# Kernel tuning notes

Measured on AMD Instinct MI355X. Metric: run time of the kernel, lower is better.

The kernel has to match this reference:

```python
import jax, jax.numpy as jnp
import numpy as np

N = 100_000   # nodes
E = 1_600_000 # edges per edge type
DIN = 128     # input_dim
DH = 128      # prot_hidden_dim
L = 3         # prot_num_layers
EPS = 1e-5


def setup_inputs() -> dict:
    key = jax.random.key(0)
    ks = jax.random.split(key, 8)
    s = 1.0 / np.sqrt(DH)
    return {
        "x": jax.random.normal(ks[0], (N, DIN), jnp.float32),
        "src": jax.random.randint(ks[1], (3, E), 0, N, jnp.int32),
        "dst": jax.random.randint(ks[2], (3, E), 0, N, jnp.int32),
        "gc_W0": jax.random.normal(ks[3], (3, DIN, DH), jnp.float32) * s,
        "gc_b0": jnp.zeros((3, DH), jnp.float32),
        "gc_W": jax.random.normal(ks[4], (L - 1, 3, DH, DH), jnp.float32) * s,
        "gc_b": jnp.zeros((L - 1, 3, DH), jnp.float32),
        "fc_W": jax.random.normal(ks[5], (L, DH, DH), jnp.float32) * s,
        "fc_b": jnp.zeros((L, DH), jnp.float32),
        "bn_gamma": jnp.ones((L, DH), jnp.float32),
        "bn_beta": jnp.zeros((L, DH), jnp.float32),
    }


def _graph_conv(x, src, dst, W, b):
    # DGL GraphConv, norm='both': D_in^{-1/2} A D_out^{-1/2} X W + b
    ones = jnp.ones(src.shape[0], x.dtype)
    deg_out = jnp.clip(jax.ops.segment_sum(ones, src, num_segments=N), 1.0)
    deg_in = jnp.clip(jax.ops.segment_sum(ones, dst, num_segments=N), 1.0)
    # apply weight first (same math; keeps gathered message width = DH)
    h = (x * jax.lax.rsqrt(deg_out)[:, None]) @ W  # [N, DH]
    agg = jax.ops.segment_sum(h[src], dst, num_segments=N)  # gather + scatter-add
    return agg * jax.lax.rsqrt(deg_in)[:, None] + b


def _batchnorm(x, gamma, beta):
    # training-mode BatchNorm1d: biased batch statistics
    mu = jnp.mean(x, axis=0)
    var = jnp.mean(jnp.square(x - mu), axis=0)
    return (x - mu) * jax.lax.rsqrt(var + EPS) * gamma + beta


def reference(x, src, dst, gc_W0, gc_b0, gc_W, gc_b, fc_W, fc_b, bn_gamma, bn_beta):
    h = x
    for l in range(L):
        W = gc_W0 if l == 0 else gc_W[l - 1]
        b = gc_b0 if l == 0 else gc_b[l - 1]
        # HeteroGraphConv with aggregate='sum' over 3 edge types
        out = _graph_conv(h, src[0], dst[0], W[0], b[0])
        for e in range(1, 3):
            out = out + _graph_conv(h, src[e], dst[e], W[e], b[e])
        # FC -> ReLU -> BatchNorm (dropout = identity in eval mode)
        h = _batchnorm(jax.nn.relu(out @ fc_W[l] + fc_b[l]), bn_gamma[l], bn_beta[l])
    return h
```

## Files before the change

### kernel.cpp

```cpp
#include <hip/hip_runtime.h>


#define EPSV 1e-5f
#define CH 4096
#define MAXNB 512

typedef __attribute__((ext_vector_type(8))) short s8v;
typedef __attribute__((ext_vector_type(4))) float f4v;

__global__ void coarse_hist(const int* __restrict__ src, const int* __restrict__ dst,
                            int* __restrict__ chd, int* __restrict__ chs,
                            int E, int NB) {
    __shared__ int hd[MAXNB], hs[MAXNB];
    int t = blockIdx.y;
    for (int i = threadIdx.x; i < MAXNB; i += 256) { hd[i] = 0; hs[i] = 0; }
    __syncthreads();
    int base = blockIdx.x * CH;
    int end = base + CH < E ? base + CH : E;
    const int* sp = src + (size_t)t * E;
    const int* dp = dst + (size_t)t * E;
    for (int i = base + threadIdx.x; i < end; i += 256) {
        atomicAdd(&hd[dp[i] >> 8], 1);
        atomicAdd(&hs[sp[i] >> 8], 1);
    }
    __syncthreads();
    for (int b = threadIdx.x; b < NB; b += 256) {
        if (hd[b]) atomicAdd(&chd[t * NB + b], hd[b]);
        if (hs[b]) atomicAdd(&chs[t * NB + b], hs[b]);
    }
}

__global__ void scan_off(const int* __restrict__ chd, const int* __restrict__ chs,
                         int* __restrict__ offd, int* __restrict__ offs,
                         int* __restrict__ gcd, int* __restrict__ gcs,
                         int* __restrict__ rowptr, int NB, int N, int E) {
    __shared__ int s[MAXNB];
    int tid = threadIdx.x;
    for (int a = 0; a < 6; ++a) {
        const int* h = (a < 3) ? chd + a * NB : chs + (a - 3) * NB;
        int* off = (a < 3) ? offd + a * (NB + 1) : offs + (a - 3) * (NB + 1);
        int* gc = (a < 3) ? gcd + a * NB : gcs + (a - 3) * NB;
        s[tid] = (tid < NB) ? h[tid] : 0;
        __syncthreads();
        for (int o = 1; o < MAXNB; o <<= 1) {
            int v = (tid >= o) ? s[tid - o] : 0;
            __syncthreads();
            s[tid] += v;
            __syncthreads();
        }
        if (tid < NB) {
            off[tid + 1] = s[tid];
            if (tid == 0) off[0] = 0;
        }
        __syncthreads();
        if (tid < NB) gc[tid] = off[tid];
        __syncthreads();
    }
    if (tid < 3) rowptr[tid * (N + 1) + N] = E;
}

__launch_bounds__(256)
__global__ void scatter_coarse(const int* __restrict__ src, const int* __restrict__ dst,
                               int* __restrict__ gcd, int* __restrict__ gcs,
                               int* __restrict__ dbuf, unsigned char* __restrict__ sbuf,
                               int E, int NB) {
    __shared__ int hd[MAXNB], hs[MAXNB];
    __shared__ int lod[MAXNB], los[MAXNB];
    __shared__ int bd[MAXNB], bs[MAXNB];
    __shared__ int rbi[CH];
    __shared__ unsigned char rbs[CH];
    const int tid = threadIdx.x;
    const int t = blockIdx.y;
    const int base = blockIdx.x * CH;
    const int end = base + CH < E ? base + CH : E;
    const int cnt = end - base;
    const int* sp = src + (size_t)t * E;
    const int* dp = dst + (size_t)t * E;

    for (int i = tid; i < MAXNB; i += 256) { hd[i] = 0; hs[i] = 0; }
    __syncthreads();
    for (int i = base + tid; i < end; i += 256) {
        atomicAdd(&hd[dp[i] >> 8], 1);
        atomicAdd(&hs[sp[i] >> 8], 1);
    }
    __syncthreads();
    for (int b = tid; b < NB; b += 256) {
        bd[b] = hd[b] ? atomicAdd(&gcd[t * NB + b], hd[b]) : 0;
        bs[b] = hs[b] ? atomicAdd(&gcs[t * NB + b], hs[b]) : 0;
    }
    lod[tid] = hd[tid]; lod[tid + 256] = hd[tid + 256];
    los[tid] = hs[tid]; los[tid + 256] = hs[tid + 256];
    __syncthreads();
    for (int o = 1; o < MAXNB; o <<= 1) {
        int a0 = lod[tid], a1 = lod[tid + 256];
        int b0 = los[tid], b1 = los[tid + 256];
        int p0 = (tid >= o) ? lod[tid - o] : 0;
        int p1 = lod[tid + 256 - o];
        int q0 = (tid >= o) ? los[tid - o] : 0;
        int q1 = los[tid + 256 - o];
        __syncthreads();
        lod[tid] = a0 + p0; lod[tid + 256] = a1 + p1;
        los[tid] = b0 + q0; los[tid + 256] = b1 + q1;
        __syncthreads();
    }
    hd[tid] = lod[tid] - hd[tid]; hd[tid + 256] = lod[tid + 256] - hd[tid + 256];
    hs[tid] = los[tid] - hs[tid]; hs[tid + 256] = los[tid + 256] - hs[tid + 256];
    __syncthreads();
    for (int i = base + tid; i < end; i += 256) {
        int sv = sp[i], dv = dp[i];
        int lp = atomicAdd(&hd[dv >> 8], 1);
        rbi[lp] = (sv << 8) | (dv & 255);
        int ls = atomicAdd(&hs[sv >> 8], 1);
        rbs[ls] = (unsigned char)(sv & 255);
    }
    __syncthreads();
    for (int i = tid; i < cnt; i += 256) {
        int lo = 0, hi = NB - 1;
        while (lo < hi) { int mid = (lo + hi) >> 1; if (lod[mid] > i) hi = mid; else lo = mid + 1; }
        int excl = lo ? lod[lo - 1] : 0;
        dbuf[(size_t)t * E + bd[lo] + (i - excl)] = rbi[i];
    }
    for (int i = tid; i < cnt; i += 256) {
        int lo = 0, hi = NB - 1;
        while (lo < hi) { int mid = (lo + hi) >> 1; if (los[mid] > i) hi = mid; else lo = mid + 1; }
        int excl = lo ? los[lo - 1] : 0;
        sbuf[(size_t)t * E + bs[lo] + (i - excl)] = rbs[i];
    }
}

__global__ void fine_src(const unsigned char* __restrict__ sbuf, const int* __restrict__ offs,
                         float* __restrict__ dro, int E, int N, int NB) {
    __shared__ int h[256];
    int b = blockIdx.x, t = blockIdx.y;
    int tid = threadIdx.x;
    h[tid] = 0;
    __syncthreads();
    int beg = offs[t * (NB + 1) + b], end = offs[t * (NB + 1) + b + 1];
    const unsigned char* sp = sbuf + (size_t)t * E;
    for (int i = beg + tid; i < end; i += 256) atomicAdd(&h[sp[i]], 1);
    __syncthreads();
    int node = b * 256 + tid;
    if (node < N) {
        int dg = h[tid] < 1 ? 1 : h[tid];
        dro[(size_t)t * N + node] = rsqrtf((float)dg);
    }
}

#define FDCAP 6656
__global__ void fine_dst(const int* __restrict__ dbuf, const int* __restrict__ offd,
                         const float* __restrict__ dro, int* __restrict__ erec,
                         int* __restrict__ rowptr, float* __restrict__ dri,
                         int E, int N, int NB) {
    __shared__ int h[256], sc[256], cur[256];
    __shared__ int rb[FDCAP];
    int b = blockIdx.x, t = blockIdx.y;
    int tid = threadIdx.x;
    h[tid] = 0;
    __syncthreads();
    int beg = offd[t * (NB + 1) + b], end = offd[t * (NB + 1) + b + 1];
    int cnt = end - beg;
    const int* dp = dbuf + (size_t)t * E;
    const float* drt = dro + (size_t)t * N;
    for (int i = beg + tid; i < end; i += 256) atomicAdd(&h[dp[i] & 255], 1);
    __syncthreads();
    sc[tid] = h[tid];
    __syncthreads();
    for (int o = 1; o < 256; o <<= 1) {
        int v = (tid >= o) ? sc[tid - o] : 0;
        __syncthreads();
        sc[tid] += v;
        __syncthreads();
    }
    int excl = sc[tid] - h[tid];
    cur[tid] = excl;
    int node = b * 256 + tid;
    if (node < N) {
        rowptr[t * (N + 1) + node] = beg + excl;
        int dg = h[tid] < 1 ? 1 : h[tid];
        dri[(size_t)t * N + node] = rsqrtf((float)dg);
    }
    __syncthreads();
    if (cnt <= FDCAP) {
        for (int i = beg + tid; i < end; i += 256) {
            int v = dp[i];
            int p = atomicAdd(&cur[v & 255], 1);
            rb[p] = v >> 8;
        }
        __syncthreads();
        for (int i = tid; i < cnt; i += 256) {
            int sv = rb[i];
            int wq = (int)(drt[sv] * 4095.0f + 0.5f);
            erec[(size_t)t * E + beg + i] = sv | (wq << 20);
        }
    } else {
        for (int i = beg + tid; i < end; i += 256) {
            int v = dp[i];
            int sv = v >> 8;
            int wq = (int)(drt[sv] * 4095.0f + 0.5f);
            int p = beg + atomicAdd(&cur[v & 255], 1);
            erec[(size_t)t * E + p] = sv | (wq << 20);
        }
    }
}

__device__ __forceinline__ unsigned int bfr(float f) {
    unsigned int u = __float_as_uint(f);
    return (u + 0x7FFFu + ((u >> 16) & 1u)) >> 16;
}
__device__ __forceinline__ unsigned int pack2(float lo, float hi) {
    return bfr(lo) | (bfr(hi) << 16);
}
__device__ __forceinline__ float blo(unsigned int u) { return __uint_as_float(u << 16); }
__device__ __forceinline__ float bhi(unsigned int u) { return __uint_as_float(u & 0xFFFF0000u); }

__global__ void cvt_bf16(const float* __restrict__ h, unsigned short* __restrict__ h2,
                         int total8) {
    int i = blockIdx.x * 256 + threadIdx.x;
    if (i >= total8) return;
    const float4* hp = (const float4*)h + (size_t)i * 2;
    float4 v0 = hp[0], v1 = hp[1];
    uint4 o;
    o.x = pack2(v0.x, v0.y);
    o.y = pack2(v0.z, v0.w);
    o.z = pack2(v1.x, v1.y);
    o.w = pack2(v1.z, v1.w);
    ((uint4*)h2)[i] = o;
}

__global__ void pack_w(const float* __restrict__ gcW0, const float* __restrict__ gcW,
                       const float* __restrict__ fcW, unsigned short* __restrict__ Wg,
                       unsigned short* __restrict__ Wf) {
    int mat = blockIdx.x;
    const float* srcp;
    unsigned short* dstp;
    if (mat < 9) {
        int l = mat / 3, e = mat % 3;
        srcp = (l == 0) ? gcW0 + (size_t)e * 16384
                        : gcW + ((size_t)(l - 1) * 3 + e) * 16384;
        dstp = Wg + (size_t)mat * 16384;
    } else {
        srcp = fcW + (size_t)(mat - 9) * 16384;
        dstp = Wf + (size_t)(mat - 9) * 16384;
    }
    for (int p = threadIdx.x; p < 16384; p += 256) {
        int j = p & 7;
        int ln = (p >> 3) & 63;
        int nt = (p >> 9) & 7;
        int ks = p >> 12;
        int k = ks * 32 + (ln >> 4) * 8 + j;
        int n = nt * 16 + (ln & 15);
        dstp[p] = (unsigned short)bfr(srcp[k * 128 + n]);
    }
}

template <int AFF>
__launch_bounds__(256)
__global__ void agg_kernel(const unsigned short* __restrict__ h2, const int* __restrict__ rowptrB,
                           const int* __restrict__ erecB, const float* __restrict__ driB,
                           const float* __restrict__ bnsum, const float* __restrict__ gamma,
                           const float* __restrict__ beta, float invn,
                           unsigned short* __restrict__ zB, int N, int E) {
    __shared__ float lss[256];
    if (AFF) {
        int tid = threadIdx.x;
        if (tid < 128) {
            float mean = bnsum[tid] * invn;
            float var = bnsum[128 + tid] * invn - mean * mean;
            float sc = gamma[tid] * rsqrtf(var + EPSV);
            lss[tid] = sc;
            lss[128 + tid] = beta[tid] - mean * sc;
        }
        __syncthreads();
    }
    const int e = blockIdx.y;
    const int* rowptr = rowptrB + e * (N + 1);
    const int* erec = erecB + (size_t)e * E;
    const float* dri = driB + (size_t)e * N;
    unsigned short* z = zB + (size_t)e * N * 128;

    int idx = blockIdx.x * 256 + threadIdx.x;
    int node = idx >> 4;
    int lq = idx & 15;
    if (node >= N) return;
    int beg = rowptr[node], end = rowptr[node + 1];
    const uint4* hp = (const uint4*)h2 + lq;
    float a0 = 0.f, a1 = 0.f, a2 = 0.f, a3 = 0.f, a4 = 0.f, a5 = 0.f, a6 = 0.f, a7 = 0.f;
    float wacc = 0.f;
    const float IW = 1.0f / 4095.0f;

    int j = beg;
    for (; j + 16 <= end; j += 16) {
        int r[16];
#pragma unroll
        for (int q = 0; q < 16; ++q) r[q] = erec[j + q];
        uint4 u[16];
#pragma unroll
        for (int q = 0; q < 16; ++q) u[q] = hp[(size_t)(r[q] & 0xFFFFF) * 16];
#pragma unroll
        for (int q = 0; q < 16; ++q) {
            float w = (float)((unsigned)r[q] >> 20) * IW;
            if (AFF) wacc += w;
            a0 += w * blo(u[q].x); a1 += w * bhi(u[q].x);
            a2 += w * blo(u[q].y); a3 += w * bhi(u[q].y);
            a4 += w * blo(u[q].z); a5 += w * bhi(u[q].z);
            a6 += w * blo(u[q].w); a7 += w * bhi(u[q].w);
        }
    }
    for (; j + 4 <= end; j += 4) {
        int r[4];
#pragma unroll
        for (int q = 0; q < 4; ++q) r[q] = erec[j + q];
        uint4 u[4];
#pragma unroll
        for (int q = 0; q < 4; ++q) u[q] = hp[(size_t)(r[q] & 0xFFFFF) * 16];
#pragma unroll
        for (int q = 0; q < 4; ++q) {
            float w = (float)((unsigned)r[q] >> 20) * IW;
            if (AFF) wacc += w;
            a0 += w * blo(u[q].x); a1 += w * bhi(u[q].x);
            a2 += w * blo(u[q].y); a3 += w * bhi(u[q].y);
            a4 += w * blo(u[q].z); a5 += w * bhi(u[q].z);
            a6 += w * blo(u[q].w); a7 += w * bhi(u[q].w);
        }
    }
    for (; j < end; ++j) {
        int r0 = erec[j];
        float w = (float)((unsigned)r0 >> 20) * IW;
        if (AFF) wacc += w;
        uint4 u0 = hp[(size_t)(r0 & 0xFFFFF) * 16];
        a0 += w * blo(u0.x); a1 += w * bhi(u0.x);
        a2 += w * blo(u0.y); a3 += w * bhi(u0.y);
        a4 += w * blo(u0.z); a5 += w * bhi(u0.z);
        a6 += w * blo(u0.w); a7 += w * bhi(u0.w);
    }
    float scl = dri[node];
    if (AFF) {
        const float* ap = &lss[lq * 8];
        const float* bp = &lss[128 + lq * 8];
        a0 = ap[0] * a0 + bp[0] * wacc;
        a1 = ap[1] * a1 + bp[1] * wacc;
        a2 = ap[2] * a2 + bp[2] * wacc;
        a3 = ap[3] * a3 + bp[3] * wacc;
        a4 = ap[4] * a4 + bp[4] * wacc;
        a5 = ap[5] * a5 + bp[5] * wacc;
        a6 = ap[6] * a6 + bp[6] * wacc;
        a7 = ap[7] * a7 + bp[7] * wacc;
    }
    uint4 o;
    o.x = pack2(a0 * scl, a1 * scl);
    o.y = pack2(a2 * scl, a3 * scl);
    o.z = pack2(a4 * scl, a5 * scl);
    o.w = pack2(a6 * scl, a7 * scl);
    ((uint4*)z)[(size_t)node * 16 + lq] = o;
}

template <int MODE>
__launch_bounds__(256)
__global__ void mfma_layer(const unsigned short* __restrict__ zB,
                           const unsigned short* __restrict__ Wgp,
                           const float* __restrict__ b3,
                           const unsigned short* __restrict__ Wfp,
                           const float* __restrict__ fcb,
                           unsigned short* __restrict__ outb, float* __restrict__ outf,
                           float* __restrict__ bnsum, int M) {
    __shared__ unsigned short T[128 * 128];
    __shared__ float red[256];
    const int tid = threadIdx.x;
    const int l = tid & 63;
    const int wv = tid >> 6;
    const int wm = wv >> 1, wn = wv & 1;
    const int m0 = blockIdx.x * 128;
    const int lr = l & 15;
    const int lk = (l >> 4) * 8;

    int rowb[4];
#pragma unroll
    for (int mt = 0; mt < 4; ++mt) {
        int r = m0 + wm * 64 + mt * 16 + lr;
        rowb[mt] = (r < M) ? r : (M - 1);
    }

    {
        f4v acc[4][4];
#pragma unroll
        for (int i = 0; i < 4; ++i)
#pragma unroll
            for (int j = 0; j < 4; ++j) acc[i][j] = (f4v){0.f, 0.f, 0.f, 0.f};
#pragma unroll
        for (int e = 0; e < 3; ++e) {
            const unsigned short* zp = zB + (size_t)e * M * 128;
            const unsigned short* wp = Wgp + (size_t)e * 16384;
#pragma unroll
            for (int ks = 0; ks < 4; ++ks) {
                s8v a[4], b[4];
#pragma unroll
                for (int mt = 0; mt < 4; ++mt)
                    a[mt] = *(const s8v*)(zp + (size_t)rowb[mt] * 128 + ks * 32 + lk);
#pragma unroll
                for (int nt = 0; nt < 4; ++nt)
                    b[nt] = *(const s8v*)(wp + ks * 4096 + (wn * 4 + nt) * 512 + l * 8);
#pragma unroll
                for (int mt = 0; mt < 4; ++mt)
#pragma unroll
                    for (int nt = 0; nt < 4; ++nt)
                        acc[mt][nt] = __builtin_amdgcn_mfma_f32_16x16x32_bf16(
                            a[mt], b[nt], acc[mt][nt], 0, 0, 0);
            }
        }
        float bs[4];
        int col[4];
#pragma unroll
        for (int nt = 0; nt < 4; ++nt) {
            col[nt] = wn * 64 + nt * 16 + lr;
            bs[nt] = b3[col[nt]] + b3[128 + col[nt]] + b3[256 + col[nt]];
        }
#pragma unroll
        for (int mt = 0; mt < 4; ++mt) {
#pragma unroll
            for (int r = 0; r < 4; ++r) {
                int rl = wm * 64 + mt * 16 + (l >> 4) * 4 + r;
#pragma unroll
                for (int nt = 0; nt < 4; ++nt) {
                    int c = col[nt];
                    int chunk = (c >> 3) ^ (rl & 15);
                    T[rl * 128 + chunk * 8 + (c & 7)] =
                        (unsigned short)bfr(acc[mt][nt][r] + bs[nt]);
                }
            }
        }
    }
    __syncthreads();

    f4v acc2[4][4];
#pragma unroll
    for (int i = 0; i < 4; ++i)
#pragma unroll
        for (int j = 0; j < 4; ++j) acc2[i][j] = (f4v){0.f, 0.f, 0.f, 0.f};
#pragma unroll
    for (int ks = 0; ks < 4; ++ks) {
        s8v a[4], b[4];
#pragma unroll
        for (int mt = 0; mt < 4; ++mt) {
            int rl = wm * 64 + mt * 16 + lr;
            int chunk = (ks * 4 + (l >> 4)) ^ lr;
            a[mt] = *(const s8v*)&T[rl * 128 + chunk * 8];
        }
#pragma unroll
        for (int nt = 0; nt < 4; ++nt)
            b[nt] = *(const s8v*)(Wfp + ks * 4096 + (wn * 4 + nt) * 512 + l * 8);
#pragma unroll
        for (int mt = 0; mt < 4; ++mt)
#pragma unroll
            for (int nt = 0; nt < 4; ++nt)
                acc2[mt][nt] = __builtin_amdgcn_mfma_f32_16x16x32_bf16(
                    a[mt], b[nt], acc2[mt][nt], 0, 0, 0);
    }

    float bv[4], cs[4] = {}, cq[4] = {};
    int col[4];
#pragma unroll
    for (int nt = 0; nt < 4; ++nt) {
        col[nt] = wn * 64 + nt * 16 + lr;
        bv[nt] = fcb[col[nt]];
    }
#pragma unroll
    for (int mt = 0; mt < 4; ++mt) {
#pragma unroll
        for (int r = 0; r < 4; ++r) {
            int row = m0 + wm * 64 + mt * 16 + (l >> 4) * 4 + r;
            if (row < M) {
#pragma unroll
                for (int nt = 0; nt < 4; ++nt) {
                    float v = acc2[mt][nt][r] + bv[nt];
                    v = v > 0.f ? v : 0.f;
                    cs[nt] += v;
                    cq[nt] += v * v;
                    if (MODE == 0)
                        outb[(size_t)row * 128 + col[nt]] = (unsigned short)bfr(v);
                    else
                        outf[(size_t)row * 128 + col[nt]] = v;
                }
            }
        }
    }
    red[tid] = 0.f;
    __syncthreads();
#pragma unroll
    for (int nt = 0; nt < 4; ++nt) {
        atomicAdd(&red[col[nt]], cs[nt]);
        atomicAdd(&red[128 + col[nt]], cq[nt]);
    }
    __syncthreads();
    if (tid < 128) {
        atomicAdd(&bnsum[tid], red[tid]);
        atomicAdd(&bnsum[128 + tid], red[128 + tid]);
    }
}

__global__ void bn_apply(float* __restrict__ h, const float* __restrict__ bnsum,
                         const float* __restrict__ gamma, const float* __restrict__ beta,
                         float invn, int total4) {
    __shared__ float lss[256];
    int tid = threadIdx.x;
    if (tid < 128) {
        float mean = bnsum[tid] * invn;
        float var = bnsum[128 + tid] * invn - mean * mean;
        float sc = gamma[tid] * rsqrtf(var + EPSV);
        lss[tid] = sc;
        lss[128 + tid] = beta[tid] - mean * sc;
    }
    __syncthreads();
    int i = blockIdx.x * 256 + tid;
    if (i >= total4) return;
    int c4 = (i & 31) * 4;
    float4 sc = *(const float4*)&lss[c4];
    float4 sh = *(const float4*)&lss[128 + c4];
    float4 v = ((float4*)h)[i];
    v.x = v.x * sc.x + sh.x;
    v.y = v.y * sc.y + sh.y;
    v.z = v.z * sc.z + sh.z;
    v.w = v.w * sc.w + sh.w;
    ((float4*)h)[i] = v;
}

extern "C" void kernel_launch(void* const* d_in, const int* in_sizes, int n_in,
                              void* d_out, int out_size, void* d_ws, size_t ws_size,
                              hipStream_t stream) {
    const float* x    = (const float*)d_in[0];
    const int*   src  = (const int*)d_in[1];
    const int*   dst  = (const int*)d_in[2];
    const float* gcW0 = (const float*)d_in[3];
    const float* gcb0 = (const float*)d_in[4];
    const float* gcW  = (const float*)d_in[5];
    const float* gcb  = (const float*)d_in[6];
    const float* fcW  = (const float*)d_in[7];
    const float* fcb  = (const float*)d_in[8];
    const float* bng  = (const float*)d_in[9];
    const float* bnb  = (const float*)d_in[10];
    float* out = (float*)d_out;

    const int N = in_sizes[0] / 128;
    const int E = in_sizes[1] / 3;
    const int NB = (N + 255) / 256;

    char* w = (char*)d_ws;
    auto alloc = [&](size_t bytes) -> char* {
        char* p = w;
        w += (bytes + 255) & ~(size_t)255;
        return p;
    };
    unsigned short* zB    = (unsigned short*)alloc((size_t)3 * N * 128 * 2);
    unsigned short* h2    = (unsigned short*)alloc((size_t)N * 128 * 2);
    unsigned short* Wg    = (unsigned short*)alloc((size_t)9 * 16384 * 2);
    unsigned short* Wf    = (unsigned short*)alloc((size_t)3 * 16384 * 2);
    int*   erec   = (int*)alloc((size_t)3 * E * 4);
    int*   rowptr = (int*)alloc((size_t)3 * (N + 1) * 4);
    float* dro    = (float*)alloc((size_t)3 * N * 4);
    float* dri    = (float*)alloc((size_t)3 * N * 4);
    int*   chd    = (int*)alloc((size_t)3 * NB * 4);
    int*   chs    = (int*)alloc((size_t)3 * NB * 4);
    int*   offd   = (int*)alloc((size_t)3 * (NB + 1) * 4);
    int*   offs   = (int*)alloc((size_t)3 * (NB + 1) * 4);
    int*   gcd    = (int*)alloc((size_t)3 * NB * 4);
    int*   gcs    = (int*)alloc((size_t)3 * NB * 4);
    float* bnsum  = (float*)alloc(256 * 4);
    int* dbuf = (int*)zB;
    unsigned char* sbuf = (unsigned char*)(dbuf + (size_t)3 * E);

    hipMemsetAsync(chd, 0, (size_t)3 * NB * 4, stream);
    hipMemsetAsync(chs, 0, (size_t)3 * NB * 4, stream);
    dim3 cg2((E + CH - 1) / CH, 3);
    coarse_hist<<<cg2, 256, 0, stream>>>(src, dst, chd, chs, E, NB);
    scan_off<<<1, MAXNB, 0, stream>>>(chd, chs, offd, offs, gcd, gcs, rowptr, NB, N, E);
    scatter_coarse<<<cg2, 256, 0, stream>>>(src, dst, gcd, gcs, dbuf, sbuf, E, NB);
    dim3 fg(NB, 3);
    fine_src<<<fg, 256, 0, stream>>>(sbuf, offs, dro, E, N, NB);
    fine_dst<<<fg, 256, 0, stream>>>(dbuf, offd, dro, erec, rowptr, dri, E, N, NB);

    pack_w<<<12, 256, 0, stream>>>(gcW0, gcW, fcW, Wg, Wf);
    const int cvtGrid = (N * 16 + 255) / 256;
    cvt_bf16<<<cvtGrid, 256, 0, stream>>>(x, h2, N * 16);

    const int gemmGrid = (N + 127) / 128;
    const float invn = 1.0f / (float)N;
    dim3 aggG((N * 16 + 255) / 256, 3);

    for (int l = 0; l < 3; ++l) {
        const float* bl = (l == 0) ? gcb0 : gcb + (size_t)(l - 1) * 3 * 128;
        if (l == 0)
            agg_kernel<0><<<aggG, 256, 0, stream>>>(h2, rowptr, erec, dri,
                                                    nullptr, nullptr, nullptr, invn,
                                                    zB, N, E);
        else
            agg_kernel<1><<<aggG, 256, 0, stream>>>(h2, rowptr, erec, dri,
                                                    bnsum, bng + (size_t)(l - 1) * 128,
                                                    bnb + (size_t)(l - 1) * 128, invn,
                                                    zB, N, E);
        hipMemsetAsync(bnsum, 0, 256 * 4, stream);
        if (l < 2)
            mfma_layer<0><<<gemmGrid, 256, 0, stream>>>(zB, Wg + (size_t)l * 3 * 16384, bl,
                                                        Wf + (size_t)l * 16384,
                                                        fcb + (size_t)l * 128,
                                                        h2, nullptr, bnsum, N);
        else
            mfma_layer<1><<<gemmGrid, 256, 0, stream>>>(zB, Wg + (size_t)l * 3 * 16384, bl,
                                                        Wf + (size_t)l * 16384,
                                                        fcb + (size_t)l * 128,
                                                        nullptr, out, bnsum, N);
    }
    bn_apply<<<(N * 32 + 255) / 256, 256, 0, stream>>>(out, bnsum, bng + 2 * 128,
                                                       bnb + 2 * 128, invn, N * 32);
}
```

Baseline: 927.8 us.

## Degree-sort nodes for aggregation and split GEMM tile across eight waves

Adds a histogram, scan and scatter pass that builds a per-edge-type node permutation sorted by in-degree. The aggregation kernel then walks nodes in that order, so the 16-lane groups sharing a wavefront have similar edge counts and less divergent loop trip counts; its main gather loop is also unrolled by 8 instead of 16. The fused MFMA layer kernel now launches 512 threads per 128-row block, with each wave computing 32 rows instead of 64, which halves accumulator registers per wave and raises the number of waves per block. The cost is three extra small preprocessing kernels, scattered writes to z in permuted order, and a reduction stage that now relies on only the first 256 threads.

Result: slower. 1.408 ms (+51.8%).

```diff
diff --git a/kernel.cpp b/kernel.cpp
--- a/kernel.cpp
+++ b/kernel.cpp
@@ -203,6 +203,50 @@
     }
 }
 
+__global__ void deg_hist(const int* __restrict__ rowptr, int* __restrict__ dhist, int N) {
+    __shared__ int h[256];
+    int t = blockIdx.y, tid = threadIdx.x;
+    h[tid] = 0;
+    __syncthreads();
+    int i = blockIdx.x * 256 + tid;
+    if (i < N) {
+        int d = rowptr[t * (N + 1) + i + 1] - rowptr[t * (N + 1) + i];
+        if (d > 255) d = 255;
+        atomicAdd(&h[d], 1);
+    }
+    __syncthreads();
+    if (h[tid]) atomicAdd(&dhist[t * 256 + tid], h[tid]);
+}
+
+__global__ void deg_scan(const int* __restrict__ dhist, int* __restrict__ dcur) {
+    __shared__ int s[256];
+    int tid = threadIdx.x;
+    for (int t = 0; t < 3; ++t) {
+        int v0 = dhist[t * 256 + tid];
+        s[tid] = v0;
+        __syncthreads();
+        for (int o = 1; o < 256; o <<= 1) {
+            int v = (tid >= o) ? s[tid - o] : 0;
+            __syncthreads();
+            s[tid] += v;
+            __syncthreads();
+        }
+        dcur[t * 256 + tid] = s[tid] - v0;
+        __syncthreads();
+    }
+}
+
+__global__ void deg_scatter(const int* __restrict__ rowptr, int* __restrict__ dcur,
+                            int* __restrict__ perm, int N) {
+    int t = blockIdx.y;
+    int i = blockIdx.x * 256 + threadIdx.x;
+    if (i >= N) return;
+    int d = rowptr[t * (N + 1) + i + 1] - rowptr[t * (N + 1) + i];
+    if (d > 255) d = 255;
+    int pos = atomicAdd(&dcur[t * 256 + d], 1);
+    perm[(size_t)t * N + pos] = i;
+}
+
 __device__ __forceinline__ unsigned int bfr(float f) {
     unsigned int u = __float_as_uint(f);
     return (u + 0x7FFFu + ((u >> 16) & 1u)) >> 16;
@@ -257,6 +301,7 @@
 __launch_bounds__(256)
 __global__ void agg_kernel(const unsigned short* __restrict__ h2, const int* __restrict__ rowptrB,
                            const int* __restrict__ erecB, const float* __restrict__ driB,
+                           const int* __restrict__ permB,
                            const float* __restrict__ bnsum, const float* __restrict__ gamma,
                            const float* __restrict__ beta, float invn,
                            unsigned short* __restrict__ zB, int N, int E) {
@@ -279,9 +324,10 @@
     unsigned short* z = zB + (size_t)e * N * 128;
 
     int idx = blockIdx.x * 256 + threadIdx.x;
-    int node = idx >> 4;
+    int g = idx >> 4;
     int lq = idx & 15;
-    if (node >= N) return;
+    if (g >= N) return;
+    int node = permB[(size_t)e * N + g];
     int beg = rowptr[node], end = rowptr[node + 1];
     const uint4* hp = (const uint4*)h2 + lq;
     float a0 = 0.f, a1 = 0.f, a2 = 0.f, a3 = 0.f, a4 = 0.f, a5 = 0.f, a6 = 0.f, a7 = 0.f;
@@ -289,15 +335,15 @@
     const float IW = 1.0f / 4095.0f;
 
     int j = beg;
-    for (; j + 16 <= end; j += 16) {
-        int r[16];
-#pragma unroll
-        for (int q = 0; q < 16; ++q) r[q] = erec[j + q];
-        uint4 u[16];
-#pragma unroll
-        for (int q = 0; q < 16; ++q) u[q] = hp[(size_t)(r[q] & 0xFFFFF) * 16];
-#pragma unroll
-        for (int q = 0; q < 16; ++q) {
+    for (; j + 8 <= end; j += 8) {
+        int r[8];
+#pragma unroll
+        for (int q = 0; q < 8; ++q) r[q] = erec[j + q];
+        uint4 u[8];
+#pragma unroll
+        for (int q = 0; q < 8; ++q) u[q] = hp[(size_t)(r[q] & 0xFFFFF) * 16];
+#pragma unroll
+        for (int q = 0; q < 8; ++q) {
             float w = (float)((unsigned)r[q] >> 20) * IW;
             if (AFF) wacc += w;
             a0 += w * blo(u[q].x); a1 += w * bhi(u[q].x);
@@ -355,7 +401,7 @@
 }
 
 template <int MODE>
-__launch_bounds__(256)
+__launch_bounds__(512)
 __global__ void mfma_layer(const unsigned short* __restrict__ zB,
                            const unsigned short* __restrict__ Wgp,
                            const float* __restrict__ b3,
@@ -368,22 +414,23 @@
     const int tid = threadIdx.x;
     const int l = tid & 63;
     const int wv = tid >> 6;
-    const int wm = wv >> 1, wn = wv & 1;
+    const int wm = wv >> 1;
+    const int wn = wv & 1;
     const int m0 = blockIdx.x * 128;
     const int lr = l & 15;
     const int lk = (l >> 4) * 8;
 
-    int rowb[4];
-#pragma unroll
-    for (int mt = 0; mt < 4; ++mt) {
-        int r = m0 + wm * 64 + mt * 16 + lr;
+    int rowb[2];
+#pragma unroll
+    for (int mt = 0; mt < 2; ++mt) {
+        int r = m0 + wm * 32 + mt * 16 + lr;
         rowb[mt] = (r < M) ? r : (M - 1);
     }
 
     {
-        f4v acc[4][4];
-#pragma unroll
-        for (int i = 0; i < 4; ++i)
+        f4v acc[2][4];
+#pragma unroll
+        for (int i = 0; i < 2; ++i)
 #pragma unroll
             for (int j = 0; j < 4; ++j) acc[i][j] = (f4v){0.f, 0.f, 0.f, 0.f};
 #pragma unroll
@@ -392,15 +439,15 @@
             const unsigned short* wp = Wgp + (size_t)e * 16384;
 #pragma unroll
             for (int ks = 0; ks < 4; ++ks) {
-                s8v a[4], b[4];
-#pragma unroll
-                for (int mt = 0; mt < 4; ++mt)
+                s8v a[2], b[4];
+#pragma unroll
+                for (int mt = 0; mt < 2; ++mt)
                     a[mt] = *(const s8v*)(zp + (size_t)rowb[mt] * 128 + ks * 32 + lk);
 #pragma unroll
                 for (int nt = 0; nt < 4; ++nt)
                     b[nt] = *(const s8v*)(wp + ks * 4096 + (wn * 4 + nt) * 512 + l * 8);
 #pragma unroll
-                for (int mt = 0; mt < 4; ++mt)
+                for (int mt = 0; mt < 2; ++mt)
 #pragma unroll
                     for (int nt = 0; nt < 4; ++nt)
                         acc[mt][nt] = __builtin_amdgcn_mfma_f32_16x16x32_bf16(
@@ -415,10 +462,10 @@
             bs[nt] = b3[col[nt]] + b3[128 + col[nt]] + b3[256 + col[nt]];
         }
 #pragma unroll
-        for (int mt = 0; mt < 4; ++mt) {
+        for (int mt = 0; mt < 2; ++mt) {
 #pragma unroll
             for (int r = 0; r < 4; ++r) {
-                int rl = wm * 64 + mt * 16 + (l >> 4) * 4 + r;
+                int rl = wm * 32 + mt * 16 + (l >> 4) * 4 + r;
 #pragma unroll
                 for (int nt = 0; nt < 4; ++nt) {
                     int c = col[nt];
@@ -431,17 +478,17 @@
     }
     __syncthreads();
 
-    f4v acc2[4][4];
-#pragma unroll
-    for (int i = 0; i < 4; ++i)
+    f4v acc2[2][4];
+#pragma unroll
+    for (int i = 0; i < 2; ++i)
 #pragma unroll
         for (int j = 0; j < 4; ++j) acc2[i][j] = (f4v){0.f, 0.f, 0.f, 0.f};
 #pragma unroll
     for (int ks = 0; ks < 4; ++ks) {
-        s8v a[4], b[4];
-#pragma unroll
-        for (int mt = 0; mt < 4; ++mt) {
-            int rl = wm * 64 + mt * 16 + lr;
+        s8v a[2], b[4];
+#pragma unroll
+        for (int mt = 0; mt < 2; ++mt) {
+            int rl = wm * 32 + mt * 16 + lr;
             int chunk = (ks * 4 + (l >> 4)) ^ lr;
             a[mt] = *(const s8v*)&T[rl * 128 + chunk * 8];
         }
@@ -449,7 +496,7 @@
         for (int nt = 0; nt < 4; ++nt)
             b[nt] = *(const s8v*)(Wfp + ks * 4096 + (wn * 4 + nt) * 512 + l * 8);
 #pragma unroll
-        for (int mt = 0; mt < 4; ++mt)
+        for (int mt = 0; mt < 2; ++mt)
 #pragma unroll
             for (int nt = 0; nt < 4; ++nt)
                 acc2[mt][nt] = __builtin_amdgcn_mfma_f32_16x16x32_bf16(
@@ -464,10 +511,10 @@
         bv[nt] = fcb[col[nt]];
     }
 #pragma unroll
-    for (int mt = 0; mt < 4; ++mt) {
+    for (int mt = 0; mt < 2; ++mt) {
 #pragma unroll
         for (int r = 0; r < 4; ++r) {
-            int row = m0 + wm * 64 + mt * 16 + (l >> 4) * 4 + r;
+            int row = m0 + wm * 32 + mt * 16 + (l >> 4) * 4 + r;
             if (row < M) {
 #pragma unroll
                 for (int nt = 0; nt < 4; ++nt) {
@@ -483,7 +530,7 @@
             }
         }
     }
-    red[tid] = 0.f;
+    if (tid < 256) red[tid] = 0.f;
     __syncthreads();
 #pragma unroll
     for (int nt = 0; nt < 4; ++nt) {
@@ -542,6 +589,7 @@
     const int N = in_sizes[0] / 128;
     const int E = in_sizes[1] / 3;
     const int NB = (N + 255) / 256;
+    const int nch = (N + 255) / 256;
 
     char* w = (char*)d_ws;
     auto alloc = [&](size_t bytes) -> char* {
@@ -557,18 +605,22 @@
     int*   rowptr = (int*)alloc((size_t)3 * (N + 1) * 4);
     float* dro    = (float*)alloc((size_t)3 * N * 4);
     float* dri    = (float*)alloc((size_t)3 * N * 4);
+    int*   perm   = (int*)alloc((size_t)3 * N * 4);
     int*   chd    = (int*)alloc((size_t)3 * NB * 4);
     int*   chs    = (int*)alloc((size_t)3 * NB * 4);
     int*   offd   = (int*)alloc((size_t)3 * (NB + 1) * 4);
     int*   offs   = (int*)alloc((size_t)3 * (NB + 1) * 4);
     int*   gcd    = (int*)alloc((size_t)3 * NB * 4);
     int*   gcs    = (int*)alloc((size_t)3 * NB * 4);
+    int*   dhist  = (int*)alloc((size_t)3 * 256 * 4);
+    int*   dcur   = (int*)alloc((size_t)3 * 256 * 4);
     float* bnsum  = (float*)alloc(256 * 4);
     int* dbuf = (int*)zB;
     unsigned char* sbuf = (unsigned char*)(dbuf + (size_t)3 * E);
 
     hipMemsetAsync(chd, 0, (size_t)3 * NB * 4, stream);
     hipMemsetAsync(chs, 0, (size_t)3 * NB * 4, stream);
+    hipMemsetAsync(dhist, 0, (size_t)3 * 256 * 4, stream);
     dim3 cg2((E + CH - 1) / CH, 3);
     coarse_hist<<<cg2, 256, 0, stream>>>(src, dst, chd, chs, E, NB);
     scan_off<<<1, MAXNB, 0, stream>>>(chd, chs, offd, offs, gcd, gcs, rowptr, NB, N, E);
@@ -577,6 +629,11 @@
     fine_src<<<fg, 256, 0, stream>>>(sbuf, offs, dro, E, N, NB);
     fine_dst<<<fg, 256, 0, stream>>>(dbuf, offd, dro, erec, rowptr, dri, E, N, NB);
 
+    dim3 dg(nch, 3);
+    deg_hist<<<dg, 256, 0, stream>>>(rowptr, dhist, N);
+    deg_scan<<<1, 256, 0, stream>>>(dhist, dcur);
+    deg_scatter<<<dg, 256, 0, stream>>>(rowptr, dcur, perm, N);
+
     pack_w<<<12, 256, 0, stream>>>(gcW0, gcW, fcW, Wg, Wf);
     const int cvtGrid = (N * 16 + 255) / 256;
     cvt_bf16<<<cvtGrid, 256, 0, stream>>>(x, h2, N * 16);
@@ -588,22 +645,22 @@
     for (int l = 0; l < 3; ++l) {
         const float* bl = (l == 0) ? gcb0 : gcb + (size_t)(l - 1) * 3 * 128;
         if (l == 0)
-            agg_kernel<0><<<aggG, 256, 0, stream>>>(h2, rowptr, erec, dri,
+            agg_kernel<0><<<aggG, 256, 0, stream>>>(h2, rowptr, erec, dri, perm,
                                                     nullptr, nullptr, nullptr, invn,
                                                     zB, N, E);
         else
-            agg_kernel<1><<<aggG, 256, 0, stream>>>(h2, rowptr, erec, dri,
+            agg_kernel<1><<<aggG, 256, 0, stream>>>(h2, rowptr, erec, dri, perm,
                                                     bnsum, bng + (size_t)(l - 1) * 128,
                                                     bnb + (size_t)(l - 1) * 128, invn,
                                                     zB, N, E);
         hipMemsetAsync(bnsum, 0, 256 * 4, stream);
         if (l < 2)
-            mfma_layer<0><<<gemmGrid, 256, 0, stream>>>(zB, Wg + (size_t)l * 3 * 16384, bl,
+            mfma_layer<0><<<gemmGrid, 512, 0, stream>>>(zB, Wg + (size_t)l * 3 * 16384, bl,
                                                         Wf + (size_t)l * 16384,
                                                         fcb + (size_t)l * 128,
                                                         h2, nullptr, bnsum, N);
         else
-            mfma_layer<1><<<gemmGrid, 256, 0, stream>>>(zB, Wg + (size_t)l * 3 * 16384, bl,
+            mfma_layer<1><<<gemmGrid, 512, 0, stream>>>(zB, Wg + (size_t)l * 3 * 16384, bl,
                                                         Wf + (size_t)l * 16384,
                                                         fcb + (size_t)l * 128,
                                                         nullptr, out, bnsum, N);
```

## Switch activations and weights to fp16 with packed half2 accumulation in aggregation

Applied to the files above, without the earlier changes.

Replaces the bf16 storage format with fp16 for activations, weights and intermediate buffers, and uses fp16 MFMA instructions. The aggregation kernel now accumulates with packed half2 FMAs instead of eight scalar fp32 FMAs per gathered vector, and its inner unroll drops from 16 to 8 edges. The fused GEMM kernel moves to 512 threads per block, with each wave covering 32 rows instead of 64. The intent is to halve the VALU work in the gather and raise GEMM occupancy, at the cost of fp16 range limits and reduced accumulation precision in the neighbour sums.

Result: faster. 899.8 us (-3.0%).

```diff
diff --git a/kernel.cpp b/kernel.cpp
--- a/kernel.cpp
+++ b/kernel.cpp
@@ -5,7 +5,8 @@
 #define CH 4096
 #define MAXNB 512
 
-typedef __attribute__((ext_vector_type(8))) short s8v;
+typedef _Float16 h2v __attribute__((ext_vector_type(2)));
+typedef _Float16 f16x8 __attribute__((ext_vector_type(8)));
 typedef __attribute__((ext_vector_type(4))) float f4v;
 
 __global__ void coarse_hist(const int* __restrict__ src, const int* __restrict__ dst,
@@ -203,27 +204,33 @@
     }
 }
 
-__device__ __forceinline__ unsigned int bfr(float f) {
-    unsigned int u = __float_as_uint(f);
-    return (u + 0x7FFFu + ((u >> 16) & 1u)) >> 16;
-}
-__device__ __forceinline__ unsigned int pack2(float lo, float hi) {
-    return bfr(lo) | (bfr(hi) << 16);
-}
-__device__ __forceinline__ float blo(unsigned int u) { return __uint_as_float(u << 16); }
-__device__ __forceinline__ float bhi(unsigned int u) { return __uint_as_float(u & 0xFFFF0000u); }
-
-__global__ void cvt_bf16(const float* __restrict__ h, unsigned short* __restrict__ h2,
-                         int total8) {
+__device__ __forceinline__ h2v ash2(unsigned u) {
+    union { unsigned u; h2v h; } c;
+    c.u = u;
+    return c.h;
+}
+__device__ __forceinline__ unsigned packh2(float lo, float hi) {
+    union { h2v h; unsigned u; } c;
+    c.h = (h2v){(_Float16)lo, (_Float16)hi};
+    return c.u;
+}
+__device__ __forceinline__ unsigned short f16b(float f) {
+    union { _Float16 h; unsigned short s; } c;
+    c.h = (_Float16)f;
+    return c.s;
+}
+
+__global__ void cvt_f16(const float* __restrict__ h, unsigned short* __restrict__ h2,
+                        int total8) {
     int i = blockIdx.x * 256 + threadIdx.x;
     if (i >= total8) return;
     const float4* hp = (const float4*)h + (size_t)i * 2;
     float4 v0 = hp[0], v1 = hp[1];
     uint4 o;
-    o.x = pack2(v0.x, v0.y);
-    o.y = pack2(v0.z, v0.w);
-    o.z = pack2(v1.x, v1.y);
-    o.w = pack2(v1.z, v1.w);
+    o.x = packh2(v0.x, v0.y);
+    o.y = packh2(v0.z, v0.w);
+    o.z = packh2(v1.x, v1.y);
+    o.w = packh2(v1.z, v1.w);
     ((uint4*)h2)[i] = o;
 }
 
@@ -249,7 +256,7 @@
         int ks = p >> 12;
         int k = ks * 32 + (ln >> 4) * 8 + j;
         int n = nt * 16 + (ln & 15);
-        dstp[p] = (unsigned short)bfr(srcp[k * 128 + n]);
+        dstp[p] = f16b(srcp[k * 128 + n]);
     }
 }
 
@@ -284,26 +291,28 @@
     if (node >= N) return;
     int beg = rowptr[node], end = rowptr[node + 1];
     const uint4* hp = (const uint4*)h2 + lq;
-    float a0 = 0.f, a1 = 0.f, a2 = 0.f, a3 = 0.f, a4 = 0.f, a5 = 0.f, a6 = 0.f, a7 = 0.f;
+    h2v ac0 = (h2v)0, ac1 = (h2v)0, ac2 = (h2v)0, ac3 = (h2v)0;
     float wacc = 0.f;
     const float IW = 1.0f / 4095.0f;
 
     int j = beg;
-    for (; j + 16 <= end; j += 16) {
-        int r[16];
-#pragma unroll
-        for (int q = 0; q < 16; ++q) r[q] = erec[j + q];
-        uint4 u[16];
-#pragma unroll
-        for (int q = 0; q < 16; ++q) u[q] = hp[(size_t)(r[q] & 0xFFFFF) * 16];
-#pragma unroll
-        for (int q = 0; q < 16; ++q) {
-            float w = (float)((unsigned)r[q] >> 20) * IW;
-            if (AFF) wacc += w;
-            a0 += w * blo(u[q].x); a1 += w * bhi(u[q].x);
-            a2 += w * blo(u[q].y); a3 += w * bhi(u[q].y);
-            a4 += w * blo(u[q].z); a5 += w * bhi(u[q].z);
-            a6 += w * blo(u[q].w); a7 += w * bhi(u[q].w);
+    for (; j + 8 <= end; j += 8) {
+        int r[8];
+#pragma unroll
+        for (int q = 0; q < 8; ++q) r[q] = erec[j + q];
+        uint4 u[8];
+#pragma unroll
+        for (int q = 0; q < 8; ++q) u[q] = hp[(size_t)(r[q] & 0xFFFFF) * 16];
+#pragma unroll
+        for (int q = 0; q < 8; ++q) {
+            float wf = (float)((unsigned)r[q] >> 20) * IW;
+            if (AFF) wacc += wf;
+            _Float16 wh = (_Float16)wf;
+            h2v wp = (h2v){wh, wh};
+            ac0 = ash2(u[q].x) * wp + ac0;
+            ac1 = ash2(u[q].y) * wp + ac1;
+            ac2 = ash2(u[q].z) * wp + ac2;
+            ac3 = ash2(u[q].w) * wp + ac3;
         }
     }
     for (; j + 4 <= end; j += 4) {
@@ -315,24 +324,32 @@
         for (int q = 0; q < 4; ++q) u[q] = hp[(size_t)(r[q] & 0xFFFFF) * 16];
 #pragma unroll
         for (int q = 0; q < 4; ++q) {
-            float w = (float)((unsigned)r[q] >> 20) * IW;
-            if (AFF) wacc += w;
-            a0 += w * blo(u[q].x); a1 += w * bhi(u[q].x);
-            a2 += w * blo(u[q].y); a3 += w * bhi(u[q].y);
-            a4 += w * blo(u[q].z); a5 += w * bhi(u[q].z);
-            a6 += w * blo(u[q].w); a7 += w * bhi(u[q].w);
+            float wf = (float)((unsigned)r[q] >> 20) * IW;
+            if (AFF) wacc += wf;
+            _Float16 wh = (_Float16)wf;
+            h2v wp = (h2v){wh, wh};
+            ac0 = ash2(u[q].x) * wp + ac0;
+            ac1 = ash2(u[q].y) * wp + ac1;
+            ac2 = ash2(u[q].z) * wp + ac2;
+            ac3 = ash2(u[q].w) * wp + ac3;
         }
     }
     for (; j < end; ++j) {
         int r0 = erec[j];
-        float w = (float)((unsigned)r0 >> 20) * IW;
-        if (AFF) wacc += w;
+        float wf = (float)((unsigned)r0 >> 20) * IW;
+        if (AFF) wacc += wf;
+        _Float16 wh = (_Float16)wf;
+        h2v wp = (h2v){wh, wh};
         uint4 u0 = hp[(size_t)(r0 & 0xFFFFF) * 16];
-        a0 += w * blo(u0.x); a1 += w * bhi(u0.x);
-        a2 += w * blo(u0.y); a3 += w * bhi(u0.y);
-        a4 += w * blo(u0.z); a5 += w * bhi(u0.z);
-        a6 += w * blo(u0.w); a7 += w * bhi(u0.w);
-    }
+        ac0 = ash2(u0.x) * wp + ac0;
+        ac1 = ash2(u0.y) * wp + ac1;
+        ac2 = ash2(u0.z) * wp + ac2;
+        ac3 = ash2(u0.w) * wp + ac3;
+    }
+    float a0 = (float)ac0[0], a1 = (float)ac0[1];
+    float a2 = (float)ac1[0], a3 = (float)ac1[1];
+    float a4 = (float)ac2[0], a5 = (float)ac2[1];
+    float a6 = (float)ac3[0], a7 = (float)ac3[1];
     float scl = dri[node];
     if (AFF) {
         const float* ap = &lss[lq * 8];
@@ -347,15 +364,15 @@
         a7 = ap[7] * a7 + bp[7] * wacc;
     }
     uint4 o;
-    o.x = pack2(a0 * scl, a1 * scl);
-    o.y = pack2(a2 * scl, a3 * scl);
-    o.z = pack2(a4 * scl, a5 * scl);
-    o.w = pack2(a6 * scl, a7 * scl);
+    o.x = packh2(a0 * scl, a1 * scl);
+    o.y = packh2(a2 * scl, a3 * scl);
+    o.z = packh2(a4 * scl, a5 * scl);
+    o.w = packh2(a6 * scl, a7 * scl);
     ((uint4*)z)[(size_t)node * 16 + lq] = o;
 }
 
 template <int MODE>
-__launch_bounds__(256)
+__launch_bounds__(512)
 __global__ void mfma_layer(const unsigned short* __restrict__ zB,
                            const unsigned short* __restrict__ Wgp,
                            const float* __restrict__ b3,
@@ -368,22 +385,23 @@
     const int tid = threadIdx.x;
     const int l = tid & 63;
     const int wv = tid >> 6;
-    const int wm = wv >> 1, wn = wv & 1;
+    const int wm = wv >> 1;
+    const int wn = wv & 1;
     const int m0 = blockIdx.x * 128;
     const int lr = l & 15;
     const int lk = (l >> 4) * 8;
 
-    int rowb[4];
-#pragma unroll
-    for (int mt = 0; mt < 4; ++mt) {
-        int r = m0 + wm * 64 + mt * 16 + lr;
+    int rowb[2];
+#pragma unroll
+    for (int mt = 0; mt < 2; ++mt) {
+        int r = m0 + wm * 32 + mt * 16 + lr;
         rowb[mt] = (r < M) ? r : (M - 1);
     }
 
     {
-        f4v acc[4][4];
-#pragma unroll
-        for (int i = 0; i < 4; ++i)
+        f4v acc[2][4];
+#pragma unroll
+        for (int i = 0; i < 2; ++i)
 #pragma unroll
             for (int j = 0; j < 4; ++j) acc[i][j] = (f4v){0.f, 0.f, 0.f, 0.f};
 #pragma unroll
@@ -392,18 +410,18 @@
             const unsigned short* wp = Wgp + (size_t)e * 16384;
 #pragma unroll
             for (int ks = 0; ks < 4; ++ks) {
-                s8v a[4], b[4];
-#pragma unroll
-                for (int mt = 0; mt < 4; ++mt)
-                    a[mt] = *(const s8v*)(zp + (size_t)rowb[mt] * 128 + ks * 32 + lk);
+                f16x8 a[2], b[4];
+#pragma unroll
+                for (int mt = 0; mt < 2; ++mt)
+                    a[mt] = *(const f16x8*)(zp + (size_t)rowb[mt] * 128 + ks * 32 + lk);
 #pragma unroll
                 for (int nt = 0; nt < 4; ++nt)
-                    b[nt] = *(const s8v*)(wp + ks * 4096 + (wn * 4 + nt) * 512 + l * 8);
-#pragma unroll
-                for (int mt = 0; mt < 4; ++mt)
+                    b[nt] = *(const f16x8*)(wp + ks * 4096 + (wn * 4 + nt) * 512 + l * 8);
+#pragma unroll
+                for (int mt = 0; mt < 2; ++mt)
 #pragma unroll
                     for (int nt = 0; nt < 4; ++nt)
-                        acc[mt][nt] = __builtin_amdgcn_mfma_f32_16x16x32_bf16(
+                        acc[mt][nt] = __builtin_amdgcn_mfma_f32_16x16x32_f16(
                             a[mt], b[nt], acc[mt][nt], 0, 0, 0);
             }
         }
@@ -415,44 +433,43 @@
             bs[nt] = b3[col[nt]] + b3[128 + col[nt]] + b3[256 + col[nt]];
         }
 #pragma unroll
-        for (int mt = 0; mt < 4; ++mt) {
+        for (int mt = 0; mt < 2; ++mt) {
 #pragma unroll
             for (int r = 0; r < 4; ++r) {
-                int rl = wm * 64 + mt * 16 + (l >> 4) * 4 + r;
+                int rl = wm * 32 + mt * 16 + (l >> 4) * 4 + r;
 #pragma unroll
                 for (int nt = 0; nt < 4; ++nt) {
                     int c = col[nt];
                     int chunk = (c >> 3) ^ (rl & 15);
-                    T[rl * 128 + chunk * 8 + (c & 7)] =
-                        (unsigned short)bfr(acc[mt][nt][r] + bs[nt]);
+                    T[rl * 128 + chunk * 8 + (c & 7)] = f16b(acc[mt][nt][r] + bs[nt]);
                 }
             }
         }
     }
     __syncthreads();
 
-    f4v acc2[4][4];
-#pragma unroll
-    for (int i = 0; i < 4; ++i)
+    f4v acc2[2][4];
+#pragma unroll
+    for (int i = 0; i < 2; ++i)
 #pragma unroll
         for (int j = 0; j < 4; ++j) acc2[i][j] = (f4v){0.f, 0.f, 0.f, 0.f};
 #pragma unroll
     for (int ks = 0; ks < 4; ++ks) {
-        s8v a[4], b[4];
-#pragma unroll
-        for (int mt = 0; mt < 4; ++mt) {
-            int rl = wm * 64 + mt * 16 + lr;
+        f16x8 a[2], b[4];
+#pragma unroll
+        for (int mt = 0; mt < 2; ++mt) {
+            int rl = wm * 32 + mt * 16 + lr;
             int chunk = (ks * 4 + (l >> 4)) ^ lr;
-            a[mt] = *(const s8v*)&T[rl * 128 + chunk * 8];
+            a[mt] = *(const f16x8*)&T[rl * 128 + chunk * 8];
         }
 #pragma unroll
         for (int nt = 0; nt < 4; ++nt)
-            b[nt] = *(const s8v*)(Wfp + ks * 4096 + (wn * 4 + nt) * 512 + l * 8);
-#pragma unroll
-        for (int mt = 0; mt < 4; ++mt)
+            b[nt] = *(const f16x8*)(Wfp + ks * 4096 + (wn * 4 + nt) * 512 + l * 8);
+#pragma unroll
+        for (int mt = 0; mt < 2; ++mt)
 #pragma unroll
             for (int nt = 0; nt < 4; ++nt)
-                acc2[mt][nt] = __builtin_amdgcn_mfma_f32_16x16x32_bf16(
+                acc2[mt][nt] = __builtin_amdgcn_mfma_f32_16x16x32_f16(
                     a[mt], b[nt], acc2[mt][nt], 0, 0, 0);
     }
 
@@ -464,10 +481,10 @@
         bv[nt] = fcb[col[nt]];
     }
 #pragma unroll
-    for (int mt = 0; mt < 4; ++mt) {
+    for (int mt = 0; mt < 2; ++mt) {
 #pragma unroll
         for (int r = 0; r < 4; ++r) {
-            int row = m0 + wm * 64 + mt * 16 + (l >> 4) * 4 + r;
+            int row = m0 + wm * 32 + mt * 16 + (l >> 4) * 4 + r;
             if (row < M) {
 #pragma unroll
                 for (int nt = 0; nt < 4; ++nt) {
@@ -476,14 +493,14 @@
                     cs[nt] += v;
                     cq[nt] += v * v;
                     if (MODE == 0)
-                        outb[(size_t)row * 128 + col[nt]] = (unsigned short)bfr(v);
+                        outb[(size_t)row * 128 + col[nt]] = f16b(v);
                     else
                         outf[(size_t)row * 128 + col[nt]] = v;
                 }
             }
         }
     }
-    red[tid] = 0.f;
+    if (tid < 256) red[tid] = 0.f;
     __syncthreads();
 #pragma unroll
     for (int nt = 0; nt < 4; ++nt) {
@@ -579,7 +596,7 @@
 
     pack_w<<<12, 256, 0, stream>>>(gcW0, gcW, fcW, Wg, Wf);
     const int cvtGrid = (N * 16 + 255) / 256;
-    cvt_bf16<<<cvtGrid, 256, 0, stream>>>(x, h2, N * 16);
+    cvt_f16<<<cvtGrid, 256, 0, stream>>>(x, h2, N * 16);
 
     const int gemmGrid = (N + 127) / 128;
     const float invn = 1.0f / (float)N;
@@ -598,12 +615,12 @@
                                                     zB, N, E);
         hipMemsetAsync(bnsum, 0, 256 * 4, stream);
         if (l < 2)
-            mfma_layer<0><<<gemmGrid, 256, 0, stream>>>(zB, Wg + (size_t)l * 3 * 16384, bl,
+            mfma_layer<0><<<gemmGrid, 512, 0, stream>>>(zB, Wg + (size_t)l * 3 * 16384, bl,
                                                         Wf + (size_t)l * 16384,
                                                         fcb + (size_t)l * 128,
                                                         h2, nullptr, bnsum, N);
         else
-            mfma_layer<1><<<gemmGrid, 256, 0, stream>>>(zB, Wg + (size_t)l * 3 * 16384, bl,
+            mfma_layer<1><<<gemmGrid, 512, 0, stream>>>(zB, Wg + (size_t)l * 3 * 16384, bl,
                                                         Wf + (size_t)l * 16384,
                                                         fcb + (size_t)l * 128,
                                                         nullptr, out, bnsum, N);
```
